# Optimization experiments

Measured on AMD Instinct MI355X. Metric: run time of the kernel, lower is better.

## Reference

```python
import jax, jax.numpy as jnp
import numpy as np

N_NODES = 50000
N_EDGES = 800000
D_IN = 128
D_HID = 128


def _sage_conv(x, src, dst, W_l, b_l, W_r, num_nodes):
    # PyG SAGEConv (mean aggr): out = lin_l(mean_{j in N(i)} x_j) + lin_r(x_i)
    msgs = x[src]  # [E, d] irregular gather
    agg = jax.ops.segment_sum(msgs, dst, num_segments=num_nodes)  # [N, d]
    cnt = jax.ops.segment_sum(jnp.ones((dst.shape[0], 1), x.dtype), dst, num_segments=num_nodes)
    agg = agg / jnp.maximum(cnt, 1.0)  # mean over in-neighbors
    return agg @ W_l.T + b_l + x @ W_r.T


def setup_inputs() -> dict:
    key = jax.random.key(0)
    ks = jax.random.split(key, 8)
    x = jax.random.normal(ks[0], (N_NODES, D_IN), dtype=jnp.float32)
    edge_index = jax.random.randint(ks[1], (2, N_EDGES), 0, N_NODES, dtype=jnp.int64)
    s0 = 1.0 / np.sqrt(D_IN)
    s1 = 1.0 / np.sqrt(D_HID)
    return {
        "x": x,
        "edge_index": edge_index,
        "W_l0": jax.random.uniform(ks[2], (D_HID, D_IN), jnp.float32, -s0, s0),
        "b_l0": jnp.zeros((D_HID,), jnp.float32),
        "W_r0": jax.random.uniform(ks[3], (D_HID, D_IN), jnp.float32, -s0, s0),
        "W_l1": jax.random.uniform(ks[4], (D_HID, D_HID), jnp.float32, -s1, s1),
        "b_l1": jnp.zeros((D_HID,), jnp.float32),
        "W_r1": jax.random.uniform(ks[5], (D_HID, D_HID), jnp.float32, -s1, s1),
    }


def reference(x, edge_index, W_l0, b_l0, W_r0, W_l1, b_l1, W_r1):
    src, dst = edge_index[0], edge_index[1]
    n = x.shape[0]
    # layer 0 + ReLU (dropout is identity at inference)
    h = _sage_conv(x, src, dst, W_l0, b_l0, W_r0, n)
    h = jax.nn.relu(h)
    # layer 1 (no activation on last layer)
    out = _sage_conv(h, src, dst, W_l1, b_l1, W_r1, n)
    return out
```

## Files before the change

### kernel.cpp

```cpp
#include <hip/hip_runtime.h>


typedef __attribute__((ext_vector_type(8))) short short8;
typedef __attribute__((ext_vector_type(4))) float f32x4;

#define DEV __device__ __forceinline__

DEV unsigned short f2b(float f) {
  unsigned u = __builtin_bit_cast(unsigned, f);
  u += 0x7fffu + ((u >> 16) & 1u);
  return (unsigned short)(u >> 16);
}
DEV float b2f(unsigned short h) {
  unsigned u = ((unsigned)h) << 16;
  return __builtin_bit_cast(float, u);
}

constexpr int N_NODES = 50000;
constexpr int N_EDGES = 800000;
constexpr int D = 128;
constexpr int NBUCK = (N_NODES + 255) / 256;
constexpr int BCAP = 5120;
constexpr int NBIN = 784;
constexpr int EPB = (N_EDGES + NBIN - 1) / NBIN;
constexpr int NCONV = (N_NODES * D / 4) / 256;
constexpr int NPREP = (2 * 32 * 128) / 256;

__global__ __launch_bounds__(256) void setup_kernel(
    const float* __restrict__ x, unsigned short* __restrict__ xb,
    const float* __restrict__ Wl0, const float* __restrict__ Wr0,
    const float* __restrict__ Wl1, const float* __restrict__ Wr1,
    unsigned short* __restrict__ Bf,
    const int* __restrict__ src, const int* __restrict__ dst,
    int* __restrict__ g_bcnt, unsigned* __restrict__ staging) {
  __shared__ int cnt[NBUCK];
  __shared__ int cur[NBUCK];
  int bid = blockIdx.x;
  int t = threadIdx.x;

  if (bid < NBIN) {
    for (int i = t; i < NBUCK; i += 256) cnt[i] = 0;
    __syncthreads();
    int beg = bid * EPB;
    int end = min(beg + EPB, N_EDGES);
    for (int e = beg + t; e < end; e += 256) {
      atomicAdd(&cnt[dst[e] >> 8], 1);
    }
    __syncthreads();
    for (int i = t; i < NBUCK; i += 256) {
      cur[i] = atomicAdd(&g_bcnt[i], cnt[i]);
    }
    __syncthreads();
    for (int e = beg + t; e < end; e += 256) {
      int d = dst[e];
      int b = d >> 8;
      int p = atomicAdd(&cur[b], 1);
      if (p >= BCAP) p = BCAP - 1;
      staging[b * BCAP + p] = ((unsigned)(d & 255) << 16) | (unsigned)src[e];
    }
    return;
  }
  if (bid < NBIN + NCONV) {
    int i = (bid - NBIN) * 256 + t;
    f32x4 v = ((const f32x4*)x)[i];
    uint2 o;
    o.x = (unsigned)f2b(v.x) | ((unsigned)f2b(v.y) << 16);
    o.y = (unsigned)f2b(v.z) | ((unsigned)f2b(v.w) << 16);
    ((uint2*)xb)[i] = o;
    return;
  }
  int f = (bid - NBIN - NCONV) * 256 + t;
  int layer = f >> 12;
  int kchunk = (f >> 7) & 31;
  int n = f & 127;
  const float* W;
  if (layer == 0) W = (kchunk < 16) ? Wl0 : Wr0;
  else            W = (kchunk < 16) ? Wl1 : Wr1;
  int k = (kchunk & 15) * 8;
  const f32x4* row = (const f32x4*)(W + n * D + k);
  f32x4 a = row[0], b = row[1];
  uint4 pk;
  pk.x = (unsigned)f2b(a.x) | ((unsigned)f2b(a.y) << 16);
  pk.y = (unsigned)f2b(a.z) | ((unsigned)f2b(a.w) << 16);
  pk.z = (unsigned)f2b(b.x) | ((unsigned)f2b(b.y) << 16);
  pk.w = (unsigned)f2b(b.z) | ((unsigned)f2b(b.w) << 16);
  *(uint4*)(Bf + (size_t)f * 8) = pk;
}

__global__ __launch_bounds__(1024) void fill2_kernel(const unsigned* __restrict__ staging,
                                                     const int* __restrict__ g_bcnt,
                                                     int* __restrict__ offs,
                                                     int* __restrict__ csr) {
  __shared__ int cnts[256];
  __shared__ int tmp[256];
  __shared__ int hist[256];
  __shared__ int cur[256];
  __shared__ int sh_n, sh_bb;
  int b = blockIdx.x;
  int t = threadIdx.x;
  if (t < 256) {
    int c = (t < NBUCK) ? g_bcnt[t] : 0;
    cnts[t] = c;
    tmp[t] = c;
    hist[t] = 0;
  }
  __syncthreads();
  if (t < 256) {
    for (int off = 1; off < 256; off <<= 1) {
      int u = (t >= off) ? tmp[t - off] : 0;
      __syncthreads();
      tmp[t] += u;
      __syncthreads();
    }
  } else {
    for (int off = 1; off < 256; off <<= 1) { __syncthreads(); __syncthreads(); }
  }
  if (t == 0) {
    sh_n = cnts[b];
    sh_bb = tmp[b] - cnts[b];
  }
  __syncthreads();
  int n = sh_n;
  int bb = sh_bb;
  if (b == 0 && t == 0) offs[N_NODES] = N_EDGES;

  const unsigned* st = staging + b * BCAP;
  for (int e = t; e < n; e += 1024) atomicAdd(&hist[st[e] >> 16], 1);
  __syncthreads();
  if (t < 256) {
    int v = hist[t];
    tmp[t] = v;
    __syncthreads();
    for (int off = 1; off < 256; off <<= 1) {
      int u = (t >= off) ? tmp[t - off] : 0;
      __syncthreads();
      tmp[t] += u;
      __syncthreads();
    }
    int excl = tmp[t] - v;
    int node = b * 256 + t;
    if (node < N_NODES) offs[node] = bb + excl;
    cur[t] = bb + excl;
  } else {
    __syncthreads();
    for (int off = 1; off < 256; off <<= 1) { __syncthreads(); __syncthreads(); }
  }
  __syncthreads();
  for (int e = t; e < n; e += 1024) {
    unsigned pk = st[e];
    int p = atomicAdd(&cur[pk >> 16], 1);
    csr[p] = (int)(pk & 0xffffu);
  }
}

__global__ void agg_kernel(const unsigned short* __restrict__ feat,
                           const int* __restrict__ csr_src,
                           const int* __restrict__ offs,
                           unsigned short* __restrict__ out) {
  int w = (int)((blockIdx.x * blockDim.x + threadIdx.x) >> 6);
  int lane = threadIdx.x & 63;
  if (w >= N_NODES) return;
  int s = offs[w], e = offs[w + 1];
  const unsigned* f = (const unsigned*)feat;
  float ax = 0.f, ay = 0.f;
  int k = s;
  for (; k + 4 <= e; k += 4) {
    int s0 = csr_src[k], s1 = csr_src[k + 1], s2 = csr_src[k + 2], s3 = csr_src[k + 3];
    unsigned u0 = f[s0 * 64 + lane];
    unsigned u1 = f[s1 * 64 + lane];
    unsigned u2 = f[s2 * 64 + lane];
    unsigned u3 = f[s3 * 64 + lane];
    ax += b2f((unsigned short)u0) + b2f((unsigned short)u1) +
          b2f((unsigned short)u2) + b2f((unsigned short)u3);
    ay += b2f((unsigned short)(u0 >> 16)) + b2f((unsigned short)(u1 >> 16)) +
          b2f((unsigned short)(u2 >> 16)) + b2f((unsigned short)(u3 >> 16));
  }
  for (; k < e; ++k) {
    unsigned u = f[csr_src[k] * 64 + lane];
    ax += b2f((unsigned short)u);
    ay += b2f((unsigned short)(u >> 16));
  }
  float inv = 1.0f / (float)max(e - s, 1);
  unsigned o = (unsigned)f2b(ax * inv) | ((unsigned)f2b(ay * inv) << 16);
  ((unsigned*)out)[w * 64 + lane] = o;
}

__global__ __launch_bounds__(256) void gemm_kernel(
    const unsigned short* __restrict__ Aagg,
    const unsigned short* __restrict__ Afeat,
    const unsigned short* __restrict__ Bf,
    const float* __restrict__ bias,
    float* __restrict__ out_f32,
    unsigned short* __restrict__ out_bf16,
    int relu_bf16) {
  int wave = threadIdx.x >> 6;
  int lane = threadIdx.x & 63;
  int ml = lane & 15;
  int quad = lane >> 4;
  int node0 = blockIdx.x * 64 + wave * 16;

  int arow = node0 + ml;
  if (arow >= N_NODES) arow = N_NODES - 1;

  f32x4 acc[8];
#pragma unroll
  for (int t = 0; t < 8; ++t) acc[t] = (f32x4){0.f, 0.f, 0.f, 0.f};

  const short8* bf8 = (const short8*)Bf;
#pragma unroll
  for (int mat = 0; mat < 2; ++mat) {
    const unsigned short* A = mat ? Afeat : Aagg;
    const short8* arow8 = (const short8*)(A + (size_t)arow * D);
    int kbase = mat * 16;
#pragma unroll
    for (int kc = 0; kc < 4; ++kc) {
      short8 af = arow8[kc * 4 + quad];
      int kchunk = kbase + kc * 4 + quad;
      const short8* brow = bf8 + kchunk * 128;
#pragma unroll
      for (int nt = 0; nt < 8; ++nt) {
        short8 bfr = brow[nt * 16 + ml];
        acc[nt] = __builtin_amdgcn_mfma_f32_16x16x32_bf16(af, bfr, acc[nt], 0, 0, 0);
      }
    }
  }

#pragma unroll
  for (int nt = 0; nt < 8; ++nt) {
    int col = nt * 16 + ml;
    float bv = bias[col];
#pragma unroll
    for (int r = 0; r < 4; ++r) {
      int node = node0 + quad * 4 + r;
      if (node >= N_NODES) continue;
      float v = acc[nt][r] + bv;
      if (relu_bf16) {
        v = v > 0.f ? v : 0.f;
        out_bf16[(size_t)node * D + col] = f2b(v);
      } else {
        out_f32[(size_t)node * D + col] = v;
      }
    }
  }
}

extern "C" void kernel_launch(void* const* d_in, const int* in_sizes, int n_in,
                              void* d_out, int out_size, void* d_ws, size_t ws_size,
                              hipStream_t stream) {
  const float* x   = (const float*)d_in[0];
  const int*   ei  = (const int*)d_in[1];
  const float* Wl0 = (const float*)d_in[2];
  const float* bl0 = (const float*)d_in[3];
  const float* Wr0 = (const float*)d_in[4];
  const float* Wl1 = (const float*)d_in[5];
  const float* bl1 = (const float*)d_in[6];
  const float* Wr1 = (const float*)d_in[7];
  float* out = (float*)d_out;

  char* ws = (char*)d_ws;
  size_t o = 0;
  auto carve = [&](size_t bytes) {
    char* p = ws + o;
    o += bytes;
    o = (o + 255) & ~(size_t)255;
    return p;
  };
  int* offs       = (int*)carve((size_t)(N_NODES + 1) * 4);
  int* csr        = (int*)carve((size_t)N_EDGES * 4);
  int* g_bcnt     = (int*)carve((size_t)NBUCK * 4);
  unsigned* staging = (unsigned*)carve((size_t)NBUCK * BCAP * 4);
  unsigned short* Bf   = (unsigned short*)carve((size_t)2 * 32 * 128 * 8 * 2);
  unsigned short* xb   = (unsigned short*)carve((size_t)N_NODES * D * 2);
  unsigned short* aggb = (unsigned short*)carve((size_t)N_NODES * D * 2);
  unsigned short* hb   = (unsigned short*)carve((size_t)N_NODES * D * 2);

  const int* srcp = ei;
  const int* dstp = ei + N_EDGES;

  hipMemsetAsync(g_bcnt, 0, (size_t)NBUCK * 4, stream);
  setup_kernel<<<NBIN + NCONV + NPREP, 256, 0, stream>>>(
      x, xb, Wl0, Wr0, Wl1, Wr1, Bf, srcp, dstp, g_bcnt, staging);
  fill2_kernel<<<NBUCK, 1024, 0, stream>>>(staging, g_bcnt, offs, csr);

  const int GEMM_BLOCKS = (N_NODES + 63) / 64;
  agg_kernel<<<(N_NODES + 3) / 4, 256, 0, stream>>>(xb, csr, offs, aggb);
  gemm_kernel<<<GEMM_BLOCKS, 256, 0, stream>>>(aggb, xb, Bf, bl0, nullptr, hb, 1);
  agg_kernel<<<(N_NODES + 3) / 4, 256, 0, stream>>>(hb, csr, offs, aggb);
  gemm_kernel<<<GEMM_BLOCKS, 256, 0, stream>>>(aggb, hb, Bf + 32 * 128 * 8, bl1,
                                               out, nullptr, 0);
}
```

Measured before the change: 228.0 us.

## Slice bf16 features into 32-column planes for cache-local aggregation

Stores the bf16 node features, layer-0 hidden state and aggregates as four column slices of 32 values each. The aggregation kernel now runs one pass per slice, so each working set is a quarter of the full table and should fit better in L2/MALL. Inside each pass a wave loads up to 64 neighbour indices at once and shares them with shuffles; four lane groups handle different edges and are reduced at the end. The GEMM load and store addressing is updated to match. The cost is four times as many aggregation blocks and repeated index and offset reads, with 64-byte rather than 256-byte row gathers.

```diff
diff --git a/kernel.cpp b/kernel.cpp
--- a/kernel.cpp
+++ b/kernel.cpp
@@ -25,6 +25,10 @@
 constexpr int EPB = (N_EDGES + NBIN - 1) / NBIN;
 constexpr int NCONV = (N_NODES * D / 4) / 256;
 constexpr int NPREP = (2 * 32 * 128) / 256;
+
+constexpr int NSLICE = 4;
+constexpr int SLICE_BF16 = N_NODES * 32;
+constexpr int NBPS = (N_NODES + 3) / 4;
 
 __global__ __launch_bounds__(256) void setup_kernel(
     const float* __restrict__ x, unsigned short* __restrict__ xb,
@@ -66,7 +70,11 @@
     uint2 o;
     o.x = (unsigned)f2b(v.x) | ((unsigned)f2b(v.y) << 16);
     o.y = (unsigned)f2b(v.z) | ((unsigned)f2b(v.w) << 16);
-    ((uint2*)xb)[i] = o;
+    int node = i >> 5;
+    int rem = i & 31;
+    int slice = rem >> 3;
+    int wq = rem & 7;
+    ((uint2*)xb)[(size_t)slice * (N_NODES * 8) + node * 8 + wq] = o;
     return;
   }
   int f = (bid - NBIN - NCONV) * 256 + t;
@@ -153,36 +161,48 @@
   }
 }
 
-__global__ void agg_kernel(const unsigned short* __restrict__ feat,
-                           const int* __restrict__ csr_src,
-                           const int* __restrict__ offs,
-                           unsigned short* __restrict__ out) {
-  int w = (int)((blockIdx.x * blockDim.x + threadIdx.x) >> 6);
+__global__ __launch_bounds__(256) void agg_kernel(
+    const unsigned short* __restrict__ feat,
+    const int* __restrict__ csr_src,
+    const int* __restrict__ offs,
+    unsigned short* __restrict__ out) {
+  int blk = blockIdx.x;
+  int slice = blk / NBPS;
+  int w = (blk - slice * NBPS) * 4 + (threadIdx.x >> 6);
   int lane = threadIdx.x & 63;
+  int g = lane >> 4;
+  int q = lane & 15;
   if (w >= N_NODES) return;
   int s = offs[w], e = offs[w + 1];
-  const unsigned* f = (const unsigned*)feat;
+  int deg = e - s;
+  const unsigned* f = (const unsigned*)feat + (size_t)slice * (N_NODES * 16);
   float ax = 0.f, ay = 0.f;
-  int k = s;
-  for (; k + 4 <= e; k += 4) {
-    int s0 = csr_src[k], s1 = csr_src[k + 1], s2 = csr_src[k + 2], s3 = csr_src[k + 3];
-    unsigned u0 = f[s0 * 64 + lane];
-    unsigned u1 = f[s1 * 64 + lane];
-    unsigned u2 = f[s2 * 64 + lane];
-    unsigned u3 = f[s3 * 64 + lane];
-    ax += b2f((unsigned short)u0) + b2f((unsigned short)u1) +
-          b2f((unsigned short)u2) + b2f((unsigned short)u3);
-    ay += b2f((unsigned short)(u0 >> 16)) + b2f((unsigned short)(u1 >> 16)) +
-          b2f((unsigned short)(u2 >> 16)) + b2f((unsigned short)(u3 >> 16));
-  }
-  for (; k < e; ++k) {
-    unsigned u = f[csr_src[k] * 64 + lane];
-    ax += b2f((unsigned short)u);
-    ay += b2f((unsigned short)(u >> 16));
-  }
-  float inv = 1.0f / (float)max(e - s, 1);
-  unsigned o = (unsigned)f2b(ax * inv) | ((unsigned)f2b(ay * inv) << 16);
-  ((unsigned*)out)[w * 64 + lane] = o;
+  for (int c = s; c < e; c += 64) {
+    int nch = min(64, e - c);
+    int idx = 0;
+    if (lane < nch) idx = __builtin_nontemporal_load(csr_src + c + lane);
+    for (int kb = 0; kb < nch; kb += 16) {
+#pragma unroll
+      for (int j = 0; j < 4; ++j) {
+        int ke = kb + (g << 2) + j;
+        int sj = __shfl(idx, ke & 63);
+        unsigned u = 0u;
+        if (ke < nch) u = f[(unsigned)sj * 16u + q];
+        ax += b2f((unsigned short)u);
+        ay += b2f((unsigned short)(u >> 16));
+      }
+    }
+  }
+  ax += __shfl_xor(ax, 16);
+  ax += __shfl_xor(ax, 32);
+  ay += __shfl_xor(ay, 16);
+  ay += __shfl_xor(ay, 32);
+  if (lane < 16) {
+    float inv = 1.0f / (float)max(deg, 1);
+    unsigned o = (unsigned)f2b(ax * inv) | ((unsigned)f2b(ay * inv) << 16);
+    unsigned* og = (unsigned*)out + (size_t)slice * (N_NODES * 16);
+    __builtin_nontemporal_store(o, og + (size_t)w * 16 + q);
+  }
 }
 
 __global__ __launch_bounds__(256) void gemm_kernel(
@@ -210,11 +230,11 @@
 #pragma unroll
   for (int mat = 0; mat < 2; ++mat) {
     const unsigned short* A = mat ? Afeat : Aagg;
-    const short8* arow8 = (const short8*)(A + (size_t)arow * D);
     int kbase = mat * 16;
 #pragma unroll
     for (int kc = 0; kc < 4; ++kc) {
-      short8 af = arow8[kc * 4 + quad];
+      short8 af = *(const short8*)(A + (size_t)kc * SLICE_BF16 +
+                                   (size_t)arow * 32 + quad * 8);
       int kchunk = kbase + kc * 4 + quad;
       const short8* brow = bf8 + kchunk * 128;
 #pragma unroll
@@ -236,7 +256,8 @@
       float v = acc[nt][r] + bv;
       if (relu_bf16) {
         v = v > 0.f ? v : 0.f;
-        out_bf16[(size_t)node * D + col] = f2b(v);
+        out_bf16[(size_t)(nt >> 1) * SLICE_BF16 + (size_t)node * 32 + (col & 31)] =
+            f2b(v);
       } else {
         out_f32[(size_t)node * D + col] = v;
       }
@@ -283,9 +304,10 @@
   fill2_kernel<<<NBUCK, 1024, 0, stream>>>(staging, g_bcnt, offs, csr);
 
   const int GEMM_BLOCKS = (N_NODES + 63) / 64;
-  agg_kernel<<<(N_NODES + 3) / 4, 256, 0, stream>>>(xb, csr, offs, aggb);
+  const int AGG_BLOCKS = NSLICE * NBPS;
+  agg_kernel<<<AGG_BLOCKS, 256, 0, stream>>>(xb, csr, offs, aggb);
   gemm_kernel<<<GEMM_BLOCKS, 256, 0, stream>>>(aggb, xb, Bf, bl0, nullptr, hb, 1);
-  agg_kernel<<<(N_NODES + 3) / 4, 256, 0, stream>>>(hb, csr, offs, aggb);
+  agg_kernel<<<AGG_BLOCKS, 256, 0, stream>>>(hb, csr, offs, aggb);
   gemm_kernel<<<GEMM_BLOCKS, 256, 0, stream>>>(aggb, hb, Bf + 32 * 128 * 8, bl1,
                                                out, nullptr, 0);
 }
```

After: 288.3 us. +26.4%, slower.
